# Optimization experiments

Measured on AMD Instinct MI355X. Metric: run time of the kernel, lower is better.

The kernel has to match this reference:

```python
import jax, jax.numpy as jnp
import numpy as np

B, NQ, NK, D, H = 4, 512, 512, 128, 32  # batch, n_queries, n_keys, kq_size, mlp hidden


def setup_inputs() -> dict:
    key = jax.random.key(0)
    ks = jax.random.split(key, 7)
    s_in = 1.0 / np.sqrt(2 * D)
    s_h = 1.0 / np.sqrt(H)
    return {
        "keys": jax.random.normal(ks[0], (B, NK, D), dtype=jnp.float32),
        "queries": jax.random.normal(ks[1], (B, NQ, D), dtype=jnp.float32),
        # first MLP layer Linear(2D, H) split into key-half and query-half
        "Wk": jax.random.uniform(ks[2], (D, H), jnp.float32, -s_in, s_in),
        "Wq": jax.random.uniform(ks[3], (D, H), jnp.float32, -s_in, s_in),
        "b1": jax.random.uniform(ks[4], (H,), jnp.float32, -s_in, s_in),
        # second MLP layer Linear(H, 1)
        "w2": jax.random.uniform(ks[5], (H,), jnp.float32, -s_h, s_h),
        "b2": jax.random.uniform(ks[6], (), jnp.float32, -s_h, s_h),
    }


def reference(keys, queries, Wk, Wq, b1, w2, b2):
    # AdditiveScorer: logits[b,q,k] = w2 . tanh(W1 @ [keys[b,k]; queries[b,q]] + b1) + b2
    # Split the concat-linear into two GEMMs (identical math, no [B,Q,K,2D] tensor).
    kh = jnp.einsum("bkd,dh->bkh", keys, Wk)            # (B, NK, H)
    qh = jnp.einsum("bqd,dh->bqh", queries, Wq)          # (B, NQ, H)
    h = jnp.tanh(qh[:, :, None, :] + kh[:, None, :, :] + b1)  # (B, NQ, NK, H)
    logits = jnp.einsum("bqkh,h->bqk", h, w2) + b2       # (B, NQ, NK)
    attn = jax.nn.softmax(logits, axis=-1)               # softmax over keys
    context = jnp.einsum("bqk,bkd->bqd", attn, keys)     # weighted value sum (values = keys)
    return context
```

## Files before the change

kernel.cpp:

```cpp
#include <hip/hip_runtime.h>

#define B 4
#define NQ 512
#define NK 512
#define D 128
#define H 32
#define G 4
#define PS 2.8853900817779268f

__device__ __forceinline__ float rcp_f(float x)  { return __builtin_amdgcn_rcpf(x); }
__device__ __forceinline__ float exp2_f(float x) { return __builtin_amdgcn_exp2f(x); }

__device__ __forceinline__ void fma4(float4& a, const float4& v, float s) {
    a.x = fmaf(s, v.x, a.x);
    a.y = fmaf(s, v.y, a.y);
    a.z = fmaf(s, v.z, a.z);
    a.w = fmaf(s, v.w, a.w);
}

__global__ __launch_bounds__(256) void proj_kernel(
    const float* __restrict__ keys, const float* __restrict__ queries,
    const float* __restrict__ Wk, const float* __restrict__ Wq,
    const float* __restrict__ b1,
    float* __restrict__ kh_t, float* __restrict__ qh)
{
    __shared__ float xs[8][D];
    const int tid = threadIdx.x;
    const int r0 = blockIdx.x * 8;
    const bool is_q = (r0 >= B * NK);
    const float* __restrict__ X = is_q ? (queries + (size_t)(r0 - B * NK) * D)
                                       : (keys + (size_t)r0 * D);
    const float* __restrict__ W = is_q ? Wq : Wk;

    reinterpret_cast<float4*>(&xs[0][0])[tid] =
        reinterpret_cast<const float4*>(X)[tid];
    __syncthreads();

    const int lr = tid >> 5;
    const int h  = tid & 31;
    float a0 = 0.f, a1 = 0.f, a2 = 0.f, a3 = 0.f;
    const float4* x4 = reinterpret_cast<const float4*>(&xs[lr][0]);
    #pragma unroll
    for (int i = 0; i < D / 4; ++i) {
        float4 v = x4[i];
        a0 = fmaf(v.x, W[(4 * i + 0) * H + h], a0);
        a1 = fmaf(v.y, W[(4 * i + 1) * H + h], a1);
        a2 = fmaf(v.z, W[(4 * i + 2) * H + h], a2);
        a3 = fmaf(v.w, W[(4 * i + 3) * H + h], a3);
    }
    float acc = (a0 + a1) + (a2 + a3);
    if (is_q) {
        const int rq = r0 - B * NK + lr;
        qh[(size_t)rq * H + h] = acc * PS;
    } else {
        const int r = r0 + lr;
        const int b = r >> 9;
        const int k = r & (NK - 1);
        kh_t[((size_t)b * H + h) * NK + k] = (acc + b1[h]) * PS;
    }
}

__global__ __launch_bounds__(256) void attend_kernel(
    const float* __restrict__ keys,
    const float* __restrict__ kh_t,
    const float* __restrict__ qh,
    const float* __restrict__ w2,
    float* __restrict__ outp)
{
    __shared__ float u_mem[H * NK];
    __shared__ float ex_t[G][NK];
    __shared__ float qv_s[G][H];
    __shared__ float w2_s[H];

    const int tid  = threadIdx.x;
    const int lane = tid & 63;
    const int w    = tid >> 6;
    const int b    = blockIdx.x >> 7;
    const int q0   = (blockIdx.x & 127) * G;

    const float* khb = kh_t + (size_t)b * H * NK;
    {
        const float4* src = reinterpret_cast<const float4*>(khb);
        float4* dst = reinterpret_cast<float4*>(u_mem);
        #pragma unroll
        for (int i = 0; i < 16; ++i)
            dst[tid + 256 * i] = src[tid + 256 * i];
    }
    if (lane < H) {
        qv_s[w][lane] = qh[((size_t)b * NQ + q0 + w) * H + lane];
        if (w == 0) w2_s[lane] = -PS * w2[lane];
    }
    __syncthreads();

    float l[8];
    #pragma unroll
    for (int j = 0; j < 8; ++j) l[j] = 0.f;
    #pragma unroll 8
    for (int h = 0; h < H; ++h) {
        const float4* row = reinterpret_cast<const float4*>(u_mem + h * NK);
        const float4 v0 = row[lane];
        const float4 v1 = row[lane + 64];
        const float qv = qv_s[w][h];
        const float wp = w2_s[h];
        l[0] = fmaf(wp, rcp_f(1.f + exp2_f(qv + v0.x)), l[0]);
        l[1] = fmaf(wp, rcp_f(1.f + exp2_f(qv + v0.y)), l[1]);
        l[2] = fmaf(wp, rcp_f(1.f + exp2_f(qv + v0.z)), l[2]);
        l[3] = fmaf(wp, rcp_f(1.f + exp2_f(qv + v0.w)), l[3]);
        l[4] = fmaf(wp, rcp_f(1.f + exp2_f(qv + v1.x)), l[4]);
        l[5] = fmaf(wp, rcp_f(1.f + exp2_f(qv + v1.y)), l[5]);
        l[6] = fmaf(wp, rcp_f(1.f + exp2_f(qv + v1.z)), l[6]);
        l[7] = fmaf(wp, rcp_f(1.f + exp2_f(qv + v1.w)), l[7]);
    }

    float m = l[0];
    #pragma unroll
    for (int j = 1; j < 8; ++j) m = fmaxf(m, l[j]);
    #pragma unroll
    for (int off = 32; off; off >>= 1) m = fmaxf(m, __shfl_xor(m, off));
    float e[8], s = 0.f;
    #pragma unroll
    for (int j = 0; j < 8; ++j) { e[j] = exp2_f(l[j] - m); s += e[j]; }
    #pragma unroll
    for (int off = 32; off; off >>= 1) s += __shfl_xor(s, off);
    const float inv = 1.f / s;
    const float4 st0 = { e[0] * inv, e[1] * inv, e[2] * inv, e[3] * inv };
    const float4 st1 = { e[4] * inv, e[5] * inv, e[6] * inv, e[7] * inv };
    reinterpret_cast<float4*>(&ex_t[w][0])[lane]   = st0;
    reinterpret_cast<float4*>(&ex_t[w][256])[lane] = st1;
    __syncthreads();

    const int dg = tid & 31;
    const int kp = tid >> 5;
    const float4* k4 = reinterpret_cast<const float4*>(
        keys + ((size_t)b * NK + kp * 64) * D) + dg;
    const float4* e0p = reinterpret_cast<const float4*>(&ex_t[0][kp * 64]);
    const float4* e1p = reinterpret_cast<const float4*>(&ex_t[1][kp * 64]);
    const float4* e2p = reinterpret_cast<const float4*>(&ex_t[2][kp * 64]);
    const float4* e3p = reinterpret_cast<const float4*>(&ex_t[3][kp * 64]);
    float4 a0 = {0,0,0,0}, a1 = a0, a2 = a0, a3 = a0;
    #pragma unroll 4
    for (int kk4 = 0; kk4 < 16; ++kk4) {
        float ea[4], eb[4], ec[4], ed[4];
        *reinterpret_cast<float4*>(ea) = e0p[kk4];
        *reinterpret_cast<float4*>(eb) = e1p[kk4];
        *reinterpret_cast<float4*>(ec) = e2p[kk4];
        *reinterpret_cast<float4*>(ed) = e3p[kk4];
        #pragma unroll
        for (int j = 0; j < 4; ++j) {
            float4 kv = k4[(size_t)(4 * kk4 + j) * (D / 4)];
            fma4(a0, kv, ea[j]);
            fma4(a1, kv, eb[j]);
            fma4(a2, kv, ec[j]);
            fma4(a3, kv, ed[j]);
        }
    }
    float (*acc_s)[G][D] = reinterpret_cast<float(*)[G][D]>(u_mem);
    *reinterpret_cast<float4*>(&acc_s[kp][0][4 * dg]) = a0;
    *reinterpret_cast<float4*>(&acc_s[kp][1][4 * dg]) = a1;
    *reinterpret_cast<float4*>(&acc_s[kp][2][4 * dg]) = a2;
    *reinterpret_cast<float4*>(&acc_s[kp][3][4 * dg]) = a3;
    __syncthreads();

    const int o = 2 * tid;
    const int g = o >> 7;
    const int d = o & 127;
    float2 r = {0.f, 0.f};
    #pragma unroll
    for (int p = 0; p < 8; ++p) {
        float2 v = *reinterpret_cast<const float2*>(&acc_s[p][g][d]);
        r.x += v.x; r.y += v.y;
    }
    *reinterpret_cast<float2*>(&outp[((size_t)b * NQ + q0 + g) * D + d]) = r;
}

extern "C" void kernel_launch(void* const* d_in, const int* in_sizes, int n_in,
                              void* d_out, int out_size, void* d_ws, size_t ws_size,
                              hipStream_t stream) {
    const float* keys    = (const float*)d_in[0];
    const float* queries = (const float*)d_in[1];
    const float* Wk      = (const float*)d_in[2];
    const float* Wq      = (const float*)d_in[3];
    const float* b1      = (const float*)d_in[4];
    const float* w2      = (const float*)d_in[5];
    float* out = (float*)d_out;

    float* kh_t = (float*)d_ws;
    float* qh   = kh_t + (size_t)B * H * NK;

    const int proj_blocks = (B * NK + B * NQ) / 8;
    proj_kernel<<<proj_blocks, 256, 0, stream>>>(keys, queries, Wk, Wq, b1, kh_t, qh);
    attend_kernel<<<B * NQ / G, 256, 0, stream>>>(keys, kh_t, qh, w2, out);
}
```

Measured before the change: 23.65 us.

## Factor tanh exponent into per-key and per-query exp terms, read Ek from global

The projection kernel now stores exp2 of the scaled key and query projections, so the attend kernel computes 1/(1+eq*ek) with one FMA and a reciprocal instead of an add, exp2 and reciprocal per element. This moves the transcendental work from the B*NQ*NK*H inner loop into the small projection stage. The attend kernel also drops the 64KB shared-memory staging of the key projections and reads them straight from global/L2, which cuts LDS use (raising possible occupancy) and the initial copy. The cost is that the key-projection rows are re-fetched from cache by every wave, and exp2 of large arguments can overflow to inf, which still gives the right limit but is numerically riskier.

```diff
diff --git a/kernel.cpp b/kernel.cpp
--- a/kernel.cpp
+++ b/kernel.cpp
@@ -22,7 +22,7 @@
     const float* __restrict__ keys, const float* __restrict__ queries,
     const float* __restrict__ Wk, const float* __restrict__ Wq,
     const float* __restrict__ b1,
-    float* __restrict__ kh_t, float* __restrict__ qh)
+    float* __restrict__ Ek, float* __restrict__ eq)
 {
     __shared__ float xs[8][D];
     const int tid = threadIdx.x;
@@ -51,25 +51,25 @@
     float acc = (a0 + a1) + (a2 + a3);
     if (is_q) {
         const int rq = r0 - B * NK + lr;
-        qh[(size_t)rq * H + h] = acc * PS;
+        eq[(size_t)rq * H + h] = exp2_f(acc * PS);
     } else {
         const int r = r0 + lr;
         const int b = r >> 9;
         const int k = r & (NK - 1);
-        kh_t[((size_t)b * H + h) * NK + k] = (acc + b1[h]) * PS;
+        Ek[((size_t)b * H + h) * NK + k] = exp2_f((acc + b1[h]) * PS);
     }
 }
 
 __global__ __launch_bounds__(256) void attend_kernel(
     const float* __restrict__ keys,
-    const float* __restrict__ kh_t,
-    const float* __restrict__ qh,
+    const float* __restrict__ Ek,
+    const float* __restrict__ eq,
     const float* __restrict__ w2,
     float* __restrict__ outp)
 {
-    __shared__ float u_mem[H * NK];
     __shared__ float ex_t[G][NK];
-    __shared__ float qv_s[G][H];
+    __shared__ float acc_s[8][G][D];
+    __shared__ float eq_s[G][H];
     __shared__ float w2_s[H];
 
     const int tid  = threadIdx.x;
@@ -78,16 +78,8 @@
     const int b    = blockIdx.x >> 7;
     const int q0   = (blockIdx.x & 127) * G;
 
-    const float* khb = kh_t + (size_t)b * H * NK;
-    {
-        const float4* src = reinterpret_cast<const float4*>(khb);
-        float4* dst = reinterpret_cast<float4*>(u_mem);
-        #pragma unroll
-        for (int i = 0; i < 16; ++i)
-            dst[tid + 256 * i] = src[tid + 256 * i];
-    }
     if (lane < H) {
-        qv_s[w][lane] = qh[((size_t)b * NQ + q0 + w) * H + lane];
+        eq_s[w][lane] = eq[((size_t)b * NQ + q0 + w) * H + lane];
         if (w == 0) w2_s[lane] = -PS * w2[lane];
     }
     __syncthreads();
@@ -95,21 +87,21 @@
     float l[8];
     #pragma unroll
     for (int j = 0; j < 8; ++j) l[j] = 0.f;
+    const float* Ekb = Ek + (size_t)b * H * NK;
     #pragma unroll 8
     for (int h = 0; h < H; ++h) {
-        const float4* row = reinterpret_cast<const float4*>(u_mem + h * NK);
-        const float4 v0 = row[lane];
-        const float4 v1 = row[lane + 64];
-        const float qv = qv_s[w][h];
+        const float4 v0 = reinterpret_cast<const float4*>(Ekb + h * NK)[lane];
+        const float4 v1 = reinterpret_cast<const float4*>(Ekb + h * NK + 256)[lane];
+        const float ev = eq_s[w][h];
         const float wp = w2_s[h];
-        l[0] = fmaf(wp, rcp_f(1.f + exp2_f(qv + v0.x)), l[0]);
-        l[1] = fmaf(wp, rcp_f(1.f + exp2_f(qv + v0.y)), l[1]);
-        l[2] = fmaf(wp, rcp_f(1.f + exp2_f(qv + v0.z)), l[2]);
-        l[3] = fmaf(wp, rcp_f(1.f + exp2_f(qv + v0.w)), l[3]);
-        l[4] = fmaf(wp, rcp_f(1.f + exp2_f(qv + v1.x)), l[4]);
-        l[5] = fmaf(wp, rcp_f(1.f + exp2_f(qv + v1.y)), l[5]);
-        l[6] = fmaf(wp, rcp_f(1.f + exp2_f(qv + v1.z)), l[6]);
-        l[7] = fmaf(wp, rcp_f(1.f + exp2_f(qv + v1.w)), l[7]);
+        l[0] = fmaf(wp, rcp_f(fmaf(ev, v0.x, 1.f)), l[0]);
+        l[1] = fmaf(wp, rcp_f(fmaf(ev, v0.y, 1.f)), l[1]);
+        l[2] = fmaf(wp, rcp_f(fmaf(ev, v0.z, 1.f)), l[2]);
+        l[3] = fmaf(wp, rcp_f(fmaf(ev, v0.w, 1.f)), l[3]);
+        l[4] = fmaf(wp, rcp_f(fmaf(ev, v1.x, 1.f)), l[4]);
+        l[5] = fmaf(wp, rcp_f(fmaf(ev, v1.y, 1.f)), l[5]);
+        l[6] = fmaf(wp, rcp_f(fmaf(ev, v1.z, 1.f)), l[6]);
+        l[7] = fmaf(wp, rcp_f(fmaf(ev, v1.w, 1.f)), l[7]);
     }
 
     float m = l[0];
@@ -154,7 +146,6 @@
             fma4(a3, kv, ed[j]);
         }
     }
-    float (*acc_s)[G][D] = reinterpret_cast<float(*)[G][D]>(u_mem);
     *reinterpret_cast<float4*>(&acc_s[kp][0][4 * dg]) = a0;
     *reinterpret_cast<float4*>(&acc_s[kp][1][4 * dg]) = a1;
     *reinterpret_cast<float4*>(&acc_s[kp][2][4 * dg]) = a2;
@@ -184,10 +175,10 @@
     const float* w2      = (const float*)d_in[5];
     float* out = (float*)d_out;
 
-    float* kh_t = (float*)d_ws;
-    float* qh   = kh_t + (size_t)B * H * NK;
+    float* Ek = (float*)d_ws;
+    float* eq = Ek + (size_t)B * H * NK;
 
     const int proj_blocks = (B * NK + B * NQ) / 8;
-    proj_kernel<<<proj_blocks, 256, 0, stream>>>(keys, queries, Wk, Wq, b1, kh_t, qh);
-    attend_kernel<<<B * NQ / G, 256, 0, stream>>>(keys, kh_t, qh, w2, out);
+    proj_kernel<<<proj_blocks, 256, 0, stream>>>(keys, queries, Wk, Wq, b1, Ek, eq);
+    attend_kernel<<<B * NQ / G, 256, 0, stream>>>(keys, Ek, eq, w2, out);
 }
```

Result: faster. 21.39 us (-9.6%).
